# Performance work log

Measured on AMD Instinct MI355X. Metric: run time of the kernel, lower is better.

Reference implementation:

```python
import jax, jax.numpy as jnp
import numpy as np

RES = 32
EPS = 1e-06


def setup_inputs() -> dict:
    key = jax.random.key(0)
    k1, k2 = jax.random.split(key)
    features = jax.random.normal(k1, (16, 32768, 64), dtype=jnp.float32)
    # coords roughly in [-1, 1] as the docstring assumes
    coords = jax.random.uniform(k2, (16, 32768, 3), dtype=jnp.float32, minval=-1.0, maxval=1.0)
    return {"features": features, "coords": coords}


def reference(features, coords):
    R = RES
    B, N, C = features.shape
    # center and normalize coords to [0, 1]
    centered = coords - coords.mean(axis=1, keepdims=True)               # [B,N,3]
    max_norm = jnp.linalg.norm(centered, axis=2, keepdims=True).max(axis=1, keepdims=True)  # [B,1,1]
    normalized_coords = centered / (max_norm * 2 + EPS) + 0.5            # [B,N,3] in [0,1]
    # voxel indices
    vi = jnp.round(normalized_coords * (R - 1)).astype(jnp.int32)        # [B,N,3]
    idx = vi[..., 0] * (R * R) + vi[..., 1] * R + vi[..., 2]             # [B,N]
    # flatten batch into segment ids: segment = b*R^3 + idx
    flat_idx = (idx + jnp.arange(B, dtype=jnp.int32)[:, None] * (R ** 3)).reshape(-1)  # [B*N]
    sums = jax.ops.segment_sum(features.reshape(B * N, C), flat_idx,
                               num_segments=B * R ** 3).reshape(B, R ** 3, C)
    counts = jax.ops.segment_sum(jnp.ones((B * N,), features.dtype), flat_idx,
                                 num_segments=B * R ** 3).reshape(B, R ** 3, 1)
    avg = sums / jnp.maximum(counts, 1.0)                                 # [B,R^3,C]
    avg_voxel_features = avg.transpose(0, 2, 1).reshape(B, C, R, R, R)
    return avg_voxel_features, normalized_coords
```

## Files before the change

### kernel.cpp

```cpp
#include <hip/hip_runtime.h>

#define NB     16
#define NPTS   32768
#define NC     64
#define RES    32
#define R3     32768
#define EPSV   1e-6f
#define NPT    (NB * NPTS)

#define QSCALE 1048576.0f
#define QINV   (1.0f / 1048576.0f)
#define QBIAS  8388608

__global__ __launch_bounds__(1024) void stats_kernel(const float* __restrict__ coords,
                                                     float* __restrict__ stats) {
    const int b = blockIdx.x;
    const int t = threadIdx.x;
    const float* cb = coords + (size_t)b * NPTS * 3;

    double sx = 0.0, sy = 0.0, sz = 0.0;
    for (int n = t; n < NPTS; n += 1024) {
        sx += (double)cb[n * 3 + 0];
        sy += (double)cb[n * 3 + 1];
        sz += (double)cb[n * 3 + 2];
    }

    __shared__ double sd[1024];
    __shared__ float  res[3];

    sd[t] = sx; __syncthreads();
    for (int o = 512; o > 0; o >>= 1) { if (t < o) sd[t] += sd[t + o]; __syncthreads(); }
    if (t == 0) res[0] = (float)(sd[0] / (double)NPTS);
    __syncthreads();
    sd[t] = sy; __syncthreads();
    for (int o = 512; o > 0; o >>= 1) { if (t < o) sd[t] += sd[t + o]; __syncthreads(); }
    if (t == 0) res[1] = (float)(sd[0] / (double)NPTS);
    __syncthreads();
    sd[t] = sz; __syncthreads();
    for (int o = 512; o > 0; o >>= 1) { if (t < o) sd[t] += sd[t + o]; __syncthreads(); }
    if (t == 0) res[2] = (float)(sd[0] / (double)NPTS);
    __syncthreads();

    const float mx = res[0], my = res[1], mz = res[2];

    float mn = 0.0f;
    for (int n = t; n < NPTS; n += 1024) {
        float dx = cb[n * 3 + 0] - mx;
        float dy = cb[n * 3 + 1] - my;
        float dz = cb[n * 3 + 2] - mz;
        mn = fmaxf(mn, sqrtf(dx * dx + dy * dy + dz * dz));
    }
    float* sf = (float*)sd;
    sf[t] = mn; __syncthreads();
    for (int o = 512; o > 0; o >>= 1) { if (t < o) sf[t] = fmaxf(sf[t], sf[t + o]); __syncthreads(); }

    if (t == 0) {
        stats[b * 4 + 0] = mx;
        stats[b * 4 + 1] = my;
        stats[b * 4 + 2] = mz;
        stats[b * 4 + 3] = sf[0] * 2.0f + EPSV;
    }
}

__global__ __launch_bounds__(256) void scatter_packed_kernel(const float* __restrict__ features,
                                                             const float* __restrict__ coords,
                                                             const float* __restrict__ stats,
                                                             unsigned long long* __restrict__ acc,
                                                             float* __restrict__ nc_out,
                                                             unsigned* __restrict__ counts) {
    const int xcd  = blockIdx.x & 7;
    const int slot = blockIdx.x >> 3;
    const int p    = (xcd << 16) | (slot << 3) | (threadIdx.x >> 5);
    const int h    = threadIdx.x & 31;
    const int b    = p >> 15;

    const float mx = stats[b * 4 + 0];
    const float my = stats[b * 4 + 1];
    const float mz = stats[b * 4 + 2];
    const float s  = stats[b * 4 + 3];

    const float nx = (coords[(size_t)p * 3 + 0] - mx) / s + 0.5f;
    const float ny = (coords[(size_t)p * 3 + 1] - my) / s + 0.5f;
    const float nz = (coords[(size_t)p * 3 + 2] - mz) / s + 0.5f;

    int vx = (int)rintf(nx * (float)(RES - 1));
    int vy = (int)rintf(ny * (float)(RES - 1));
    int vz = (int)rintf(nz * (float)(RES - 1));
    vx = min(max(vx, 0), RES - 1);
    vy = min(max(vy, 0), RES - 1);
    vz = min(max(vz, 0), RES - 1);
    const int vox = vx * (RES * RES) + vy * RES + vz;

    if (h < 3) {
        const float v = (h == 0) ? nx : ((h == 1) ? ny : nz);
        nc_out[(size_t)p * 3 + h] = v;
    }
    if (h == 0) atomicAdd(&counts[((size_t)b << 15) + vox], 1u);

    const float2 f2 = *(const float2*)(features + ((size_t)p << 6) + (h << 1));
    const int q0 = (int)rintf(f2.x * QSCALE);
    const int q1 = (int)rintf(f2.y * QSCALE);
    const unsigned long long pk =
        (unsigned long long)(unsigned)(q0 + QBIAS) |
        ((unsigned long long)(unsigned)(q1 + QBIAS) << 32);

    atomicAdd(&acc[(((size_t)((b << 15) + vox)) << 5) + h], pk);
}

__global__ __launch_bounds__(256) void finalize_kernel(const unsigned long long* __restrict__ acc,
                                                       const unsigned* __restrict__ counts,
                                                       float* __restrict__ out0) {
    const int bkt = ((blockIdx.x & 7) << 10) | (blockIdx.x >> 3);
    const int b   = bkt >> 9;
    const int v0  = (bkt & 511) << 6;
    const int tid = threadIdx.x;

    __shared__ float    t[64][65];
    __shared__ float    rcs[64];
    __shared__ unsigned cnts[64];

    unsigned c = 0;
    if (tid < 64) {
        c = counts[((size_t)b << 15) + v0 + tid];
        cnts[tid] = c;
        rcs[tid]  = 1.0f / fmaxf((float)c, 1.0f);
    }
    const int any = __syncthreads_or(c != 0);

    float* o = out0 + ((size_t)b << 21) + v0;
    const int vl0 = (tid & 15) << 2;

    if (!any) {
        const float4 z = {0.0f, 0.0f, 0.0f, 0.0f};
#pragma unroll
        for (int k = 0; k < 4; k++) {
            const int ch = (tid >> 4) + (k << 4);
            *(float4*)(o + ((size_t)ch << 15) + vl0) = z;
        }
        return;
    }

    const unsigned long long* a = acc + (((size_t)((b << 15) + v0)) << 5);
#pragma unroll
    for (int i = 0; i < 8; i++) {
        const int f  = i * 256 + tid;
        const int v  = f >> 5;
        const int hh = f & 31;
        const unsigned long long u = a[f];
        const long long bias = (long long)cnts[v] * (long long)QBIAS;
        const long long q0 = (long long)(u & 0xffffffffull) - bias;
        const long long q1 = (long long)(u >> 32) - bias;
        const float rc = rcs[v] * QINV;
        t[v][2 * hh + 0] = (float)q0 * rc;
        t[v][2 * hh + 1] = (float)q1 * rc;
    }
    __syncthreads();

#pragma unroll
    for (int k = 0; k < 4; k++) {
        const int ch = (tid >> 4) + (k << 4);
        float4 v4;
        v4.x = t[vl0 + 0][ch];
        v4.y = t[vl0 + 1][ch];
        v4.z = t[vl0 + 2][ch];
        v4.w = t[vl0 + 3][ch];
        *(float4*)(o + ((size_t)ch << 15) + vl0) = v4;
    }
}

extern "C" void kernel_launch(void* const* d_in, const int* in_sizes, int n_in,
                              void* d_out, int out_size, void* d_ws, size_t ws_size,
                              hipStream_t stream) {
    const float* features = (const float*)d_in[0];
    const float* coords   = (const float*)d_in[1];

    float* out0   = (float*)d_out;
    float* nc_out = (float*)d_out + (size_t)NB * NC * R3;

    char* ws = (char*)d_ws;
    float*              stats  = (float*)ws;
    unsigned*           counts = (unsigned*)(ws + 4096);
    unsigned long long* acc    = (unsigned long long*)(ws + 4096 + (size_t)NB * R3 * 4);

    const size_t counts_bytes = (size_t)NB * R3 * 4;
    const size_t acc_bytes    = (size_t)NB * R3 * 32 * 8;

    hipMemsetAsync(counts, 0, counts_bytes + acc_bytes, stream);

    stats_kernel<<<NB, 1024, 0, stream>>>(coords, stats);

    scatter_packed_kernel<<<(NPT * 32) / 256, 256, 0, stream>>>(features, coords, stats,
                                                                acc, nc_out, counts);

    finalize_kernel<<<NB * 512, 256, 0, stream>>>(acc, counts, out0);
}
```

Before: 378.6 us.

## Split coordinate stats across 128 blocks and fuse workspace zeroing into kernel

Replaces the 16-block stats kernel with two kernels. The first zeroes the workspace (done counter, counts, accumulators) with a grid-stride loop and, in its first 128 blocks, computes partial coordinate sums per batch slice. The second computes per-slice max norms, and the last block to finish, found through an atomic counter, folds everything into the per-batch stats. This spreads the serial reduction over more compute units and removes the separate memset, at the cost of an extra kernel launch and a last-block serial fold.

```diff
diff --git a/kernel.cpp b/kernel.cpp
--- a/kernel.cpp
+++ b/kernel.cpp
@@ -12,53 +12,92 @@
 #define QINV   (1.0f / 1048576.0f)
 #define QBIAS  8388608
 
-__global__ __launch_bounds__(1024) void stats_kernel(const float* __restrict__ coords,
-                                                     float* __restrict__ stats) {
-    const int b = blockIdx.x;
+#define ZQUADS 8519936
+
+__global__ __launch_bounds__(256) void zero_stats_kernel(const float* __restrict__ coords,
+                                                         ulonglong2* __restrict__ zbase,
+                                                         double* __restrict__ psum) {
+    const int gtid = blockIdx.x * 256 + threadIdx.x;
+    const ulonglong2 z2 = {0ull, 0ull};
+    for (size_t i = gtid; i < ZQUADS; i += 2048 * 256) zbase[i] = z2;
+
+    if (blockIdx.x < 128) {
+        const int b = blockIdx.x >> 3, s = blockIdx.x & 7;
+        const float* cb = coords + ((size_t)b * NPTS + (size_t)s * 4096) * 3;
+
+        double sx = 0.0, sy = 0.0, sz = 0.0;
+        for (int n = threadIdx.x; n < 4096; n += 256) {
+            sx += (double)cb[n * 3 + 0];
+            sy += (double)cb[n * 3 + 1];
+            sz += (double)cb[n * 3 + 2];
+        }
+        __shared__ double sd[256];
+        const int t = threadIdx.x;
+        sd[t] = sx; __syncthreads();
+        for (int o = 128; o > 0; o >>= 1) { if (t < o) sd[t] += sd[t + o]; __syncthreads(); }
+        if (t == 0) psum[blockIdx.x * 3 + 0] = sd[0];
+        __syncthreads();
+        sd[t] = sy; __syncthreads();
+        for (int o = 128; o > 0; o >>= 1) { if (t < o) sd[t] += sd[t + o]; __syncthreads(); }
+        if (t == 0) psum[blockIdx.x * 3 + 1] = sd[0];
+        __syncthreads();
+        sd[t] = sz; __syncthreads();
+        for (int o = 128; o > 0; o >>= 1) { if (t < o) sd[t] += sd[t + o]; __syncthreads(); }
+        if (t == 0) psum[blockIdx.x * 3 + 2] = sd[0];
+    }
+}
+
+__global__ __launch_bounds__(256) void maxnorm_fold_kernel(const float* __restrict__ coords,
+                                                           const double* __restrict__ psum,
+                                                           float* __restrict__ pmax,
+                                                           unsigned* __restrict__ done,
+                                                           float* __restrict__ stats) {
+    const int blk = blockIdx.x;
+    const int b = blk >> 3, s = blk & 7;
+
+    double dx = 0.0, dy = 0.0, dz = 0.0;
+    for (int i = 0; i < 8; i++) {
+        dx += psum[(b * 8 + i) * 3 + 0];
+        dy += psum[(b * 8 + i) * 3 + 1];
+        dz += psum[(b * 8 + i) * 3 + 2];
+    }
+    const float mx = (float)(dx / (double)NPTS);
+    const float my = (float)(dy / (double)NPTS);
+    const float mz = (float)(dz / (double)NPTS);
+
+    const float* cb = coords + ((size_t)b * NPTS + (size_t)s * 4096) * 3;
+    float mn = 0.0f;
+    for (int n = threadIdx.x; n < 4096; n += 256) {
+        float ax = cb[n * 3 + 0] - mx;
+        float ay = cb[n * 3 + 1] - my;
+        float az = cb[n * 3 + 2] - mz;
+        mn = fmaxf(mn, sqrtf(ax * ax + ay * ay + az * az));
+    }
+    __shared__ float sf[256];
     const int t = threadIdx.x;
-    const float* cb = coords + (size_t)b * NPTS * 3;
-
-    double sx = 0.0, sy = 0.0, sz = 0.0;
-    for (int n = t; n < NPTS; n += 1024) {
-        sx += (double)cb[n * 3 + 0];
-        sy += (double)cb[n * 3 + 1];
-        sz += (double)cb[n * 3 + 2];
-    }
-
-    __shared__ double sd[1024];
-    __shared__ float  res[3];
-
-    sd[t] = sx; __syncthreads();
-    for (int o = 512; o > 0; o >>= 1) { if (t < o) sd[t] += sd[t + o]; __syncthreads(); }
-    if (t == 0) res[0] = (float)(sd[0] / (double)NPTS);
-    __syncthreads();
-    sd[t] = sy; __syncthreads();
-    for (int o = 512; o > 0; o >>= 1) { if (t < o) sd[t] += sd[t + o]; __syncthreads(); }
-    if (t == 0) res[1] = (float)(sd[0] / (double)NPTS);
-    __syncthreads();
-    sd[t] = sz; __syncthreads();
-    for (int o = 512; o > 0; o >>= 1) { if (t < o) sd[t] += sd[t + o]; __syncthreads(); }
-    if (t == 0) res[2] = (float)(sd[0] / (double)NPTS);
-    __syncthreads();
-
-    const float mx = res[0], my = res[1], mz = res[2];
-
-    float mn = 0.0f;
-    for (int n = t; n < NPTS; n += 1024) {
-        float dx = cb[n * 3 + 0] - mx;
-        float dy = cb[n * 3 + 1] - my;
-        float dz = cb[n * 3 + 2] - mz;
-        mn = fmaxf(mn, sqrtf(dx * dx + dy * dy + dz * dz));
-    }
-    float* sf = (float*)sd;
     sf[t] = mn; __syncthreads();
-    for (int o = 512; o > 0; o >>= 1) { if (t < o) sf[t] = fmaxf(sf[t], sf[t + o]); __syncthreads(); }
+    for (int o = 128; o > 0; o >>= 1) { if (t < o) sf[t] = fmaxf(sf[t], sf[t + o]); __syncthreads(); }
 
     if (t == 0) {
-        stats[b * 4 + 0] = mx;
-        stats[b * 4 + 1] = my;
-        stats[b * 4 + 2] = mz;
-        stats[b * 4 + 3] = sf[0] * 2.0f + EPSV;
+        pmax[blk] = sf[0];
+        __threadfence();
+        const unsigned old = atomicAdd(done, 1u);
+        if (old == 127u) {
+            __threadfence();
+            for (int bb = 0; bb < NB; bb++) {
+                double fx = 0.0, fy = 0.0, fz = 0.0; float m = 0.0f;
+                for (int i = 0; i < 8; i++) {
+                    fx += psum[(bb * 8 + i) * 3 + 0];
+                    fy += psum[(bb * 8 + i) * 3 + 1];
+                    fz += psum[(bb * 8 + i) * 3 + 2];
+                    m  = fmaxf(m, pmax[bb * 8 + i]);
+                }
+                stats[bb * 4 + 0] = (float)(fx / (double)NPTS);
+                stats[bb * 4 + 1] = (float)(fy / (double)NPTS);
+                stats[bb * 4 + 2] = (float)(fz / (double)NPTS);
+                stats[bb * 4 + 3] = m * 2.0f + EPSV;
+            }
+        }
     }
 }
 
@@ -179,18 +218,16 @@
 
     char* ws = (char*)d_ws;
     float*              stats  = (float*)ws;
-    unsigned*           counts = (unsigned*)(ws + 4096);
-    unsigned long long* acc    = (unsigned long long*)(ws + 4096 + (size_t)NB * R3 * 4);
-
-    const size_t counts_bytes = (size_t)NB * R3 * 4;
-    const size_t acc_bytes    = (size_t)NB * R3 * 32 * 8;
-
-    hipMemsetAsync(counts, 0, counts_bytes + acc_bytes, stream);
-
-    stats_kernel<<<NB, 1024, 0, stream>>>(coords, stats);
-
+    double*             psum   = (double*)(ws + 256);
+    float*              pmax   = (float*)(ws + 3584);
+    unsigned*           done   = (unsigned*)(ws + 4096);
+    ulonglong2*         zbase  = (ulonglong2*)(ws + 4096);
+    unsigned*           counts = (unsigned*)(ws + 8192);
+    unsigned long long* acc    = (unsigned long long*)(ws + 8192 + (size_t)NB * R3 * 4);
+
+    zero_stats_kernel<<<2048, 256, 0, stream>>>(coords, zbase, psum);
+    maxnorm_fold_kernel<<<128, 256, 0, stream>>>(coords, psum, pmax, done, stats);
     scatter_packed_kernel<<<(NPT * 32) / 256, 256, 0, stream>>>(features, coords, stats,
                                                                 acc, nc_out, counts);
-
     finalize_kernel<<<NB * 512, 256, 0, stream>>>(acc, counts, out0);
 }
```

Result: no change. 371.8 us (-1.8%).
